# Performance work log

Measured on AMD Instinct MI355X. Metric: run time of the kernel, lower is better.

## Reference

```python
import jax, jax.numpy as jnp
import numpy as np

N_NODES = 100000
N_EDGES = 1600000
N_GRAPHS = 1024
HID = 128
FINAL = 128
SPATIAL = 3
NUM_LAYERS = 3
VOCAB = 100


def _linear_params(key, d_in, d_out):
    k1, k2 = jax.random.split(key)
    s = 1.0 / np.sqrt(d_in)
    W = jax.random.uniform(k1, (d_out, d_in), jnp.float32, -s, s)
    b = jax.random.uniform(k2, (d_out,), jnp.float32, -s, s)
    return W, b


def setup_inputs() -> dict:
    key = jax.random.key(0)
    ks = jax.random.split(key, 16)
    z = jax.random.randint(ks[0], (N_NODES,), 0, VOCAB)
    pos = jax.random.normal(ks[1], (N_NODES, SPATIAL), jnp.float32)
    edge_index = jax.random.randint(ks[2], (2, N_EDGES), 0, N_NODES)
    batch = jnp.sort(jax.random.randint(ks[3], (N_NODES,), 0, N_GRAPHS))
    emb_table = jax.random.normal(ks[4], (VOCAB, HID), jnp.float32)
    W_pos, b_pos = _linear_params(ks[5], SPATIAL, HID)
    W_comb, b_comb = _linear_params(ks[6], 2 * HID, HID)
    # GIN: each conv's MLP is Linear(d,d) -> ReLU -> Linear(d,d); all dims 128 here.
    gW1, gb1, gW2, gb2 = [], [], [], []
    for i in range(NUM_LAYERS):
        k = jax.random.fold_in(ks[7], i)
        ka, kb = jax.random.split(k)
        W1, b1 = _linear_params(ka, HID, HID)
        W2, b2 = _linear_params(kb, HID, FINAL if i == NUM_LAYERS - 1 else HID)
        gW1.append(W1); gb1.append(b1); gW2.append(W2); gb2.append(b2)
    gin_W1 = jnp.stack(gW1); gin_b1 = jnp.stack(gb1)
    gin_W2 = jnp.stack(gW2); gin_b2 = jnp.stack(gb2)
    W_p1, b_p1 = _linear_params(ks[8], FINAL, FINAL)
    W_p2, b_p2 = _linear_params(ks[9], FINAL, 1)
    return {
        "z": z, "pos": pos, "edge_index": edge_index, "batch": batch,
        "emb_table": emb_table, "W_pos": W_pos, "b_pos": b_pos,
        "W_comb": W_comb, "b_comb": b_comb,
        "gin_W1": gin_W1, "gin_b1": gin_b1, "gin_W2": gin_W2, "gin_b2": gin_b2,
        "W_p1": W_p1, "b_p1": b_p1, "W_p2": W_p2, "b_p2": b_p2,
    }


def reference(z, pos, edge_index, batch, emb_table, W_pos, b_pos, W_comb, b_comb,
              gin_W1, gin_b1, gin_W2, gin_b2, W_p1, b_p1, W_p2, b_p2):
    src, dst = edge_index[0], edge_index[1]
    # initial node embedding: embed(z) || linear(pos) -> linear -> relu
    atom = emb_table[z]                                   # [N, H]
    pe = pos @ W_pos.T + b_pos                            # [N, H]
    x = jax.nn.relu(jnp.concatenate([atom, pe], axis=-1) @ W_comb.T + b_comb)
    # GIN layers: x' = MLP((1+eps)*x + sum_{j->i} x_j), eps=0; act between convs only
    for i in range(NUM_LAYERS):
        aggr = jax.ops.segment_sum(x[src], dst, num_segments=N_NODES)  # [N, H]
        h = aggr + x
        h = jax.nn.relu(h @ gin_W1[i].T + gin_b1[i])
        x = h @ gin_W2[i].T + gin_b2[i]
        if i < NUM_LAYERS - 1:
            x = jax.nn.relu(x)
    # sum pooling per graph, then predict MLP
    g = jax.ops.segment_sum(x, batch, num_segments=N_GRAPHS)  # [G, F]
    h = jax.nn.relu(g @ W_p1.T + b_p1)
    return h @ W_p2.T + b_p2                              # [G, 1]
```

## Files before the change

### kernel.cpp

```cpp
#include <hip/hip_runtime.h>
#include <hip/hip_bf16.h>

#define HID 128
#define CAP 64
#define NBK 2048
#define NBL 1563

typedef __attribute__((ext_vector_type(8))) short bfrag;
typedef __attribute__((ext_vector_type(4))) float f32x4;

static inline size_t align256(size_t x) { return (x + 255) & ~(size_t)255; }

__device__ __forceinline__ unsigned short f2bf(float f) {
  unsigned int x = __float_as_uint(f);
  unsigned int r = x + 0x7fffu + ((x >> 16) & 1u);
  return (unsigned short)(r >> 16);
}
__device__ __forceinline__ float bflo(unsigned int u) { return __uint_as_float(u << 16); }
__device__ __forceinline__ float bfhi(unsigned int u) { return __uint_as_float(u & 0xffff0000u); }


__global__ __launch_bounds__(256) void k_prep(const int* __restrict__ src,
                                              const int* __restrict__ dst,
                                              int* __restrict__ cnt,
                                              int* __restrict__ bsrc, int E, int N,
                                              const float* __restrict__ W_comb,
                                              const float* __restrict__ gW1,
                                              const float* __restrict__ gW2,
                                              unsigned short* __restrict__ Wcb,
                                              unsigned short* __restrict__ W1b,
                                              unsigned short* __restrict__ W2b,
                                              const int* __restrict__ batch,
                                              int* __restrict__ goff, int G) {
  const int bid = blockIdx.x;
  const int tid = threadIdx.x;
  if (bid < NBK) {
    const int slice = bid & 7;
    const int sidx = bid >> 3;
    const int s_lo = (int)(((long long)slice * N) >> 3);
    const int s_hi = (int)(((long long)(slice + 1) * N) >> 3);
    for (int e = sidx * 256 + tid; e < E; e += (NBK / 8) * 256) {
      int d = dst[e];
      if (d >= s_lo && d < s_hi) {
        int slot = atomicAdd(&cnt[d], 1);
        if (slot < CAP) bsrc[(size_t)d * CAP + slot] = src[e];
      }
    }
  } else if (bid < NBK + 192) {
    int i = (bid - NBK) * 256 + tid;
    if (i < 128 * 256) Wcb[i] = f2bf(W_comb[i]);
    if (i < 3 * 128 * 128) {
      W1b[i] = f2bf(gW1[i]);
      W2b[i] = f2bf(gW2[i]);
    }
  } else {
    int g = (bid - NBK - 192) * 256 + tid;
    if (g <= G) {
      int lo = 0, hi = N;
      while (lo < hi) {
        int mid = (lo + hi) >> 1;
        if (batch[mid] < g) lo = mid + 1; else hi = mid;
      }
      goff[g] = lo;
    }
  }
}


__global__ __launch_bounds__(256, 2) void k_init_mm(const int* __restrict__ z,
                                                    const float* __restrict__ pos,
                                                    const float* __restrict__ emb,
                                                    const float* __restrict__ W_pos,
                                                    const float* __restrict__ b_pos,
                                                    const unsigned short* __restrict__ Wcb,
                                                    const float* __restrict__ bias,
                                                    const unsigned short* __restrict__ W1n,
                                                    unsigned short* __restrict__ Y, int n) {
  __shared__ unsigned int sE[32 * 128];
  __shared__ unsigned int sB[32 * 64];
  const int t = threadIdx.x;
  const int w = t >> 6, l = t & 63, lr = l & 15, lk = l >> 4;

  bfrag wcf[2][8];
#pragma unroll
  for (int s = 0; s < 2; ++s)
#pragma unroll
    for (int ks = 0; ks < 8; ++ks)
      wcf[s][ks] = *(const bfrag*)(Wcb + (size_t)(32 * w + 16 * s + lr) * 256 + ks * 32 + lk * 8);
  bfrag w1f[2][4];
#pragma unroll
  for (int s = 0; s < 2; ++s)
#pragma unroll
    for (int ks = 0; ks < 4; ++ks)
      w1f[s][ks] = *(const bfrag*)(W1n + (size_t)(32 * w + 16 * s + lr) * HID + ks * 32 + lk * 8);
  const float bias0 = bias[32 * w + lr];
  const float bias1 = bias[32 * w + 16 + lr];

  const int m0 = blockIdx.x * 32;
  {
    const int r = t >> 3, i = t & 7;
    int node = m0 + r;
    if (node >= n) node = n - 1;
    const int zz = z[node];
    const float p0 = pos[node * 3 + 0], p1 = pos[node * 3 + 1], p2 = pos[node * 3 + 2];
    const int swz = (r & 7) << 2;
#pragma unroll
    for (int k = 0; k < 16; ++k) {
      const int j = i + k * 8;
      float v0, v1;
      if (j < 64) {
        const float2 ev = *(const float2*)&emb[(size_t)zz * 128 + 2 * j];
        v0 = ev.x; v1 = ev.y;
      } else {
        const int f0 = 2 * j - 128;
        v0 = b_pos[f0] + W_pos[f0 * 3] * p0 + W_pos[f0 * 3 + 1] * p1 + W_pos[f0 * 3 + 2] * p2;
        v1 = b_pos[f0 + 1] + W_pos[f0 * 3 + 3] * p0 + W_pos[f0 * 3 + 4] * p1 +
             W_pos[f0 * 3 + 5] * p2;
      }
      sE[r * 128 + (j ^ swz)] = (unsigned int)f2bf(v0) | ((unsigned int)f2bf(v1) << 16);
    }
  }
  __syncthreads();

  f32x4 acc00 = {0.f, 0.f, 0.f, 0.f}, acc01 = acc00, acc10 = acc00, acc11 = acc00;
#pragma unroll
  for (int mt = 0; mt < 2; ++mt) {
    const int row = 16 * mt + lr;
    const int swz = (row & 7) << 2;
#pragma unroll
    for (int ks = 0; ks < 8; ++ks) {
      const bfrag a = *(const bfrag*)&sE[row * 128 + ((ks * 16 + lk * 4) ^ swz)];
      if (mt == 0) {
        acc00 = __builtin_amdgcn_mfma_f32_16x16x32_bf16(a, wcf[0][ks], acc00, 0, 0, 0);
        acc01 = __builtin_amdgcn_mfma_f32_16x16x32_bf16(a, wcf[1][ks], acc01, 0, 0, 0);
      } else {
        acc10 = __builtin_amdgcn_mfma_f32_16x16x32_bf16(a, wcf[0][ks], acc10, 0, 0, 0);
        acc11 = __builtin_amdgcn_mfma_f32_16x16x32_bf16(a, wcf[1][ks], acc11, 0, 0, 0);
      }
    }
  }
  {
    unsigned short* sB16 = (unsigned short*)sB;
#pragma unroll
    for (int mt = 0; mt < 2; ++mt) {
#pragma unroll
      for (int s = 0; s < 2; ++s) {
        const f32x4 a = mt == 0 ? (s == 0 ? acc00 : acc01) : (s == 0 ? acc10 : acc11);
        const float bb = s == 0 ? bias0 : bias1;
        const int col = 32 * w + 16 * s + lr;
#pragma unroll
        for (int r = 0; r < 4; ++r) {
          const int rowL = 16 * mt + 4 * lk + r;
          const int cu = (col >> 1) ^ ((rowL & 7) << 2);
          sB16[rowL * 128 + cu * 2 + (col & 1)] = f2bf(fmaxf(a[r] + bb, 0.f));
        }
      }
    }
  }
  __syncthreads();

  f32x4 u00 = {0.f, 0.f, 0.f, 0.f}, u01 = u00, u10 = u00, u11 = u00;
#pragma unroll
  for (int mt = 0; mt < 2; ++mt) {
    const int row = 16 * mt + lr;
    const int swz = (row & 7) << 2;
#pragma unroll
    for (int ks = 0; ks < 4; ++ks) {
      const bfrag a = *(const bfrag*)&sB[row * 64 + ((ks * 16 + lk * 4) ^ swz)];
      if (mt == 0) {
        u00 = __builtin_amdgcn_mfma_f32_16x16x32_bf16(a, w1f[0][ks], u00, 0, 0, 0);
        u01 = __builtin_amdgcn_mfma_f32_16x16x32_bf16(a, w1f[1][ks], u01, 0, 0, 0);
      } else {
        u10 = __builtin_amdgcn_mfma_f32_16x16x32_bf16(a, w1f[0][ks], u10, 0, 0, 0);
        u11 = __builtin_amdgcn_mfma_f32_16x16x32_bf16(a, w1f[1][ks], u11, 0, 0, 0);
      }
    }
  }
#pragma unroll
  for (int mt = 0; mt < 2; ++mt) {
#pragma unroll
    for (int s = 0; s < 2; ++s) {
      const f32x4 a = mt == 0 ? (s == 0 ? u00 : u01) : (s == 0 ? u10 : u11);
      const int col = 32 * w + 16 * s + lr;
#pragma unroll
      for (int r = 0; r < 4; ++r) {
        const int row = m0 + 16 * mt + 4 * lk + r;
        if (row < n) Y[(size_t)row * HID + col] = f2bf(a[r]);
      }
    }
  }
}


template <int LAST>
__global__ __launch_bounds__(256, 2) void k_layer(const unsigned int* __restrict__ U,
                                                  const int* __restrict__ cnt,
                                                  const int* __restrict__ bsrc,
                                                  const float* __restrict__ b1,
                                                  const unsigned short* __restrict__ W2b,
                                                  const float* __restrict__ b2,
                                                  const unsigned short* __restrict__ W1n,
                                                  unsigned short* __restrict__ Y, int n) {
  __shared__ unsigned int sA[32 * 64];
  __shared__ unsigned int sB[32 * 64];
  const int t = threadIdx.x;
  const int w = t >> 6, l = t & 63, lr = l & 15, lk = l >> 4;

  bfrag w2f[2][4];
#pragma unroll
  for (int s = 0; s < 2; ++s)
#pragma unroll
    for (int ks = 0; ks < 4; ++ks)
      w2f[s][ks] = *(const bfrag*)(W2b + (size_t)(32 * w + 16 * s + lr) * HID + ks * 32 + lk * 8);
  bfrag w1f[2][4];
  if (!LAST) {
#pragma unroll
    for (int s = 0; s < 2; ++s)
#pragma unroll
      for (int ks = 0; ks < 4; ++ks)
        w1f[s][ks] = *(const bfrag*)(W1n + (size_t)(32 * w + 16 * s + lr) * HID + ks * 32 + lk * 8);
  }
  const float b2a = b2[32 * w + lr];
  const float b2b = b2[32 * w + 16 + lr];
  const float2 b1v = *(const float2*)&b1[2 * l];

  const int ntiles = (n + 31) >> 5;
  for (int tile = blockIdx.x; tile < ntiles; tile += gridDim.x) {
    const int m0 = tile * 32;
#pragma unroll 1
    for (int ri = 0; ri < 8; ++ri) {
      const int row = 8 * w + ri;
      int node = m0 + row;
      if (node >= n) node = n - 1;
      int deg = cnt[node];
      if (deg > CAP) deg = CAP;
      const int eidx = bsrc[(size_t)node * CAP + l];
      const unsigned int us = U[(size_t)node * 64 + l];
      float s0[8], s1[8];
#pragma unroll
      for (int jj = 0; jj < 8; ++jj) { s0[jj] = 0.f; s1[jj] = 0.f; }
      s0[0] = bflo(us); s1[0] = bfhi(us);
      if (deg > 0) {
        for (int k = 0; k < deg; k += 8) {
#pragma unroll
          for (int jj = 0; jj < 8; ++jj) {
            const int kk = k + jj;
            const int lane = kk < deg ? kk : deg - 1;
            const int sidx = __shfl(eidx, lane);
            const unsigned int uu = U[(size_t)sidx * 64 + l];
            const float m = kk < deg ? 1.f : 0.f;
            s0[jj] += m * bflo(uu);
            s1[jj] += m * bfhi(uu);
          }
        }
      }
      const float r0 = ((s0[0] + s0[1]) + (s0[2] + s0[3])) + ((s0[4] + s0[5]) + (s0[6] + s0[7]));
      const float r1 = ((s1[0] + s1[1]) + (s1[2] + s1[3])) + ((s1[4] + s1[5]) + (s1[6] + s1[7]));
      sA[row * 64 + (l ^ ((row & 7) << 2))] =
          (unsigned int)f2bf(fmaxf(r0 + b1v.x, 0.f)) |
          ((unsigned int)f2bf(fmaxf(r1 + b1v.y, 0.f)) << 16);
    }
    __syncthreads();

    f32x4 acc00 = {0.f, 0.f, 0.f, 0.f}, acc01 = acc00, acc10 = acc00, acc11 = acc00;
#pragma unroll
    for (int mt = 0; mt < 2; ++mt) {
      const int row = 16 * mt + lr;
      const int swz = (row & 7) << 2;
#pragma unroll
      for (int ks = 0; ks < 4; ++ks) {
        const bfrag a = *(const bfrag*)&sA[row * 64 + ((ks * 16 + lk * 4) ^ swz)];
        if (mt == 0) {
          acc00 = __builtin_amdgcn_mfma_f32_16x16x32_bf16(a, w2f[0][ks], acc00, 0, 0, 0);
          acc01 = __builtin_amdgcn_mfma_f32_16x16x32_bf16(a, w2f[1][ks], acc01, 0, 0, 0);
        } else {
          acc10 = __builtin_amdgcn_mfma_f32_16x16x32_bf16(a, w2f[0][ks], acc10, 0, 0, 0);
          acc11 = __builtin_amdgcn_mfma_f32_16x16x32_bf16(a, w2f[1][ks], acc11, 0, 0, 0);
        }
      }
    }
    if (LAST) {
#pragma unroll
      for (int mt = 0; mt < 2; ++mt) {
#pragma unroll
        for (int s = 0; s < 2; ++s) {
          const f32x4 a = mt == 0 ? (s == 0 ? acc00 : acc01) : (s == 0 ? acc10 : acc11);
          const float bb = s == 0 ? b2a : b2b;
          const int col = 32 * w + 16 * s + lr;
#pragma unroll
          for (int r = 0; r < 4; ++r) {
            const int row = m0 + 16 * mt + 4 * lk + r;
            if (row < n) Y[(size_t)row * HID + col] = f2bf(a[r] + bb);
          }
        }
      }
      __syncthreads();
    } else {
      unsigned short* sB16 = (unsigned short*)sB;
#pragma unroll
      for (int mt = 0; mt < 2; ++mt) {
#pragma unroll
        for (int s = 0; s < 2; ++s) {
          const f32x4 a = mt == 0 ? (s == 0 ? acc00 : acc01) : (s == 0 ? acc10 : acc11);
          const float bb = s == 0 ? b2a : b2b;
          const int col = 32 * w + 16 * s + lr;
#pragma unroll
          for (int r = 0; r < 4; ++r) {
            const int rowL = 16 * mt + 4 * lk + r;
            const int cu = (col >> 1) ^ ((rowL & 7) << 2);
            sB16[rowL * 128 + cu * 2 + (col & 1)] = f2bf(fmaxf(a[r] + bb, 0.f));
          }
        }
      }
      __syncthreads();
      f32x4 u00 = {0.f, 0.f, 0.f, 0.f}, u01 = u00, u10 = u00, u11 = u00;
#pragma unroll
      for (int mt = 0; mt < 2; ++mt) {
        const int row = 16 * mt + lr;
        const int swz = (row & 7) << 2;
#pragma unroll
        for (int ks = 0; ks < 4; ++ks) {
          const bfrag a = *(const bfrag*)&sB[row * 64 + ((ks * 16 + lk * 4) ^ swz)];
          if (mt == 0) {
            u00 = __builtin_amdgcn_mfma_f32_16x16x32_bf16(a, w1f[0][ks], u00, 0, 0, 0);
            u01 = __builtin_amdgcn_mfma_f32_16x16x32_bf16(a, w1f[1][ks], u01, 0, 0, 0);
          } else {
            u10 = __builtin_amdgcn_mfma_f32_16x16x32_bf16(a, w1f[0][ks], u10, 0, 0, 0);
            u11 = __builtin_amdgcn_mfma_f32_16x16x32_bf16(a, w1f[1][ks], u11, 0, 0, 0);
          }
        }
      }
#pragma unroll
      for (int mt = 0; mt < 2; ++mt) {
#pragma unroll
        for (int s = 0; s < 2; ++s) {
          const f32x4 a = mt == 0 ? (s == 0 ? u00 : u01) : (s == 0 ? u10 : u11);
          const int col = 32 * w + 16 * s + lr;
#pragma unroll
          for (int r = 0; r < 4; ++r) {
            const int row = m0 + 16 * mt + 4 * lk + r;
            if (row < n) Y[(size_t)row * HID + col] = f2bf(a[r]);
          }
        }
      }
    }
  }
}


__global__ __launch_bounds__(128) void k_pool(const unsigned short* __restrict__ X,
                                              const int* __restrict__ goff,
                                              const float* __restrict__ Wp1,
                                              const float* __restrict__ bp1,
                                              const float* __restrict__ Wp2,
                                              const float* __restrict__ bp2,
                                              float* __restrict__ out, int G) {
  __shared__ float sg[HID];
  __shared__ float sred[HID];
  int g = blockIdx.x;
  int f = threadIdx.x;
  int n0 = goff[g], n1 = goff[g + 1];
  float c0 = 0.f, c1 = 0.f, c2 = 0.f, c3 = 0.f;
  int nn = n0;
  for (; nn + 3 < n1; nn += 4) {
    c0 += __uint_as_float((unsigned int)X[(size_t)nn * HID + f] << 16);
    c1 += __uint_as_float((unsigned int)X[(size_t)(nn + 1) * HID + f] << 16);
    c2 += __uint_as_float((unsigned int)X[(size_t)(nn + 2) * HID + f] << 16);
    c3 += __uint_as_float((unsigned int)X[(size_t)(nn + 3) * HID + f] << 16);
  }
  for (; nn < n1; ++nn) c0 += __uint_as_float((unsigned int)X[(size_t)nn * HID + f] << 16);
  sg[f] = (c0 + c1) + (c2 + c3);
  __syncthreads();
  float a0 = 0.f, a1 = 0.f, a2 = 0.f, a3 = 0.f;
#pragma unroll
  for (int k4 = 0; k4 < 32; ++k4) {
    float4 wv = *(const float4*)&Wp1[f * HID + k4 * 4];
    float4 xv = *(const float4*)&sg[k4 * 4];
    a0 += wv.x * xv.x; a1 += wv.y * xv.y; a2 += wv.z * xv.z; a3 += wv.w * xv.w;
  }
  float h = fmaxf(bp1[f] + ((a0 + a1) + (a2 + a3)), 0.f);
  sred[f] = Wp2[f] * h;
  __syncthreads();
  for (int s = 64; s > 0; s >>= 1) {
    if (f < s) sred[f] += sred[f + s];
    __syncthreads();
  }
  if (f == 0) out[g] = sred[0] + bp2[0];
}


extern "C" void kernel_launch(void* const* d_in, const int* in_sizes, int n_in,
                              void* d_out, int out_size, void* d_ws, size_t ws_size,
                              hipStream_t stream) {
  const int*   z      = (const int*)d_in[0];
  const float* pos    = (const float*)d_in[1];
  const int*   ei     = (const int*)d_in[2];
  const int*   batch  = (const int*)d_in[3];
  const float* emb    = (const float*)d_in[4];
  const float* W_pos  = (const float*)d_in[5];
  const float* b_pos  = (const float*)d_in[6];
  const float* W_comb = (const float*)d_in[7];
  const float* b_comb = (const float*)d_in[8];
  const float* gW1    = (const float*)d_in[9];
  const float* gb1    = (const float*)d_in[10];
  const float* gW2    = (const float*)d_in[11];
  const float* gb2    = (const float*)d_in[12];
  const float* Wp1    = (const float*)d_in[13];
  const float* bp1    = (const float*)d_in[14];
  const float* Wp2    = (const float*)d_in[15];
  const float* bp2    = (const float*)d_in[16];
  float* out = (float*)d_out;

  const int N = in_sizes[0];
  const int E = in_sizes[2] / 2;
  const int G = out_size;
  const int* srcp = ei;
  const int* dstp = ei + E;

  char* w = (char*)d_ws;
  unsigned short* Ub  = (unsigned short*)w; w += align256((size_t)N * 128 * 2);
  unsigned short* Vb  = (unsigned short*)w; w += align256((size_t)N * 128 * 2);
  unsigned short* Wcb = (unsigned short*)w; w += align256((size_t)128 * 256 * 2);
  unsigned short* W1b = (unsigned short*)w; w += align256((size_t)3 * 128 * 128 * 2);
  unsigned short* W2b = (unsigned short*)w; w += align256((size_t)3 * 128 * 128 * 2);
  int* cnt  = (int*)w; w += align256((size_t)N * 4);
  int* bsrc = (int*)w; w += align256((size_t)N * CAP * 4);
  int* goff = (int*)w; w += align256((size_t)(G + 1) * 4);

  hipMemsetAsync(cnt, 0, (size_t)N * 4, stream);

  k_prep<<<NBK + 192 + 5, 256, 0, stream>>>(srcp, dstp, cnt, bsrc, E, N,
                                            W_comb, gW1, gW2, Wcb, W1b, W2b,
                                            batch, goff, G);

  k_init_mm<<<(N + 31) / 32, 256, 0, stream>>>(z, pos, emb, W_pos, b_pos, Wcb, b_comb,
                                               W1b, Ub, N);

  k_layer<0><<<NBL, 256, 0, stream>>>((const unsigned int*)Ub, cnt, bsrc, gb1,
                                      W2b, gb2, W1b + (size_t)1 * 128 * 128, Vb, N);
  k_layer<0><<<NBL, 256, 0, stream>>>((const unsigned int*)Vb, cnt, bsrc, gb1 + 128,
                                      W2b + (size_t)1 * 128 * 128, gb2 + 128,
                                      W1b + (size_t)2 * 128 * 128, Ub, N);
  k_layer<1><<<NBL, 256, 0, stream>>>((const unsigned int*)Ub, cnt, bsrc, gb1 + 256,
                                      W2b + (size_t)2 * 128 * 128, gb2 + 256,
                                      (const unsigned short*)nullptr, Vb, N);

  k_pool<<<G, HID, 0, stream>>>(Vb, goff, Wp1, bp1, Wp2, bp2, out, G);
}
```

Before: 476.6 us.

## Vectorize neighbor gather with 16-byte loads and four edges per wave

The aggregation loop now has each wave split into four lane groups of 16. Each lane loads a 16-byte uint4 of the bf16 row, so one wave gathers four neighbor rows per instruction, and partial sums are reduced with xor shuffles. Degrees and edge indices for all eight rows are prefetched up front. The persistent grid-stride tile loop is replaced by one block per 32-row tile, and the occupancy hint is raised from 2 to 3 blocks per CU. This targets the latency of many 4-byte scattered gathers, at the cost of extra shuffle reductions and higher register pressure.

```diff
diff --git a/kernel.cpp b/kernel.cpp
--- a/kernel.cpp
+++ b/kernel.cpp
@@ -4,7 +4,6 @@
 #define HID 128
 #define CAP 64
 #define NBK 2048
-#define NBL 1563
 
 typedef __attribute__((ext_vector_type(8))) short bfrag;
 typedef __attribute__((ext_vector_type(4))) float f32x4;
@@ -193,7 +192,7 @@
 
 
 template <int LAST>
-__global__ __launch_bounds__(256, 2) void k_layer(const unsigned int* __restrict__ U,
+__global__ __launch_bounds__(256, 3) void k_layer(const unsigned int* __restrict__ U,
                                                   const int* __restrict__ cnt,
                                                   const int* __restrict__ bsrc,
                                                   const float* __restrict__ b1,
@@ -205,6 +204,7 @@
   __shared__ unsigned int sB[32 * 64];
   const int t = threadIdx.x;
   const int w = t >> 6, l = t & 63, lr = l & 15, lk = l >> 4;
+  const int lgrp = lk, lpos = lr;
 
   bfrag w2f[2][4];
 #pragma unroll
@@ -222,125 +222,155 @@
   }
   const float b2a = b2[32 * w + lr];
   const float b2b = b2[32 * w + 16 + lr];
-  const float2 b1v = *(const float2*)&b1[2 * l];
-
-  const int ntiles = (n + 31) >> 5;
-  for (int tile = blockIdx.x; tile < ntiles; tile += gridDim.x) {
-    const int m0 = tile * 32;
-#pragma unroll 1
-    for (int ri = 0; ri < 8; ++ri) {
-      const int row = 8 * w + ri;
-      int node = m0 + row;
-      if (node >= n) node = n - 1;
-      int deg = cnt[node];
-      if (deg > CAP) deg = CAP;
-      const int eidx = bsrc[(size_t)node * CAP + l];
-      const unsigned int us = U[(size_t)node * 64 + l];
-      float s0[8], s1[8];
-#pragma unroll
-      for (int jj = 0; jj < 8; ++jj) { s0[jj] = 0.f; s1[jj] = 0.f; }
-      s0[0] = bflo(us); s1[0] = bfhi(us);
-      if (deg > 0) {
-        for (int k = 0; k < deg; k += 8) {
-#pragma unroll
-          for (int jj = 0; jj < 8; ++jj) {
-            const int kk = k + jj;
-            const int lane = kk < deg ? kk : deg - 1;
-            const int sidx = __shfl(eidx, lane);
-            const unsigned int uu = U[(size_t)sidx * 64 + l];
-            const float m = kk < deg ? 1.f : 0.f;
-            s0[jj] += m * bflo(uu);
-            s1[jj] += m * bfhi(uu);
-          }
+  const float4 bb0 = *(const float4*)&b1[8 * lpos];
+  const float4 bb1 = *(const float4*)&b1[8 * lpos + 4];
+  const float ms = (lgrp == 0) ? 1.f : 0.f;
+
+  const int m0 = blockIdx.x * 32;
+
+  int degs[8];
+  int eidxs[8];
+#pragma unroll
+  for (int ri = 0; ri < 8; ++ri) {
+    int node = m0 + 8 * w + ri;
+    if (node >= n) node = n - 1;
+    int d = cnt[node];
+    degs[ri] = d > CAP ? CAP : d;
+    eidxs[ri] = bsrc[(size_t)node * CAP + l];
+  }
+#pragma unroll
+  for (int ri = 0; ri < 8; ++ri) {
+    const int row = 8 * w + ri;
+    int node = m0 + row;
+    if (node >= n) node = n - 1;
+    const int deg = degs[ri];
+    const int eidx = eidxs[ri];
+    const uint4 sv = *(const uint4*)(U + (size_t)node * 64 + 4 * lpos);
+    float a0 = ms * bflo(sv.x), a1 = ms * bfhi(sv.x);
+    float a2 = ms * bflo(sv.y), a3 = ms * bfhi(sv.y);
+    float a4 = ms * bflo(sv.z), a5 = ms * bfhi(sv.z);
+    float a6 = ms * bflo(sv.w), a7 = ms * bfhi(sv.w);
+    int k = 0;
+    for (; k + 7 < deg; k += 8) {
+      const int e0 = __shfl(eidx, k + lgrp);
+      const int e1 = __shfl(eidx, k + 4 + lgrp);
+      const uint4 u0 = *(const uint4*)(U + (size_t)e0 * 64 + 4 * lpos);
+      const uint4 u1 = *(const uint4*)(U + (size_t)e1 * 64 + 4 * lpos);
+      a0 += bflo(u0.x); a1 += bfhi(u0.x); a2 += bflo(u0.y); a3 += bfhi(u0.y);
+      a4 += bflo(u0.z); a5 += bfhi(u0.z); a6 += bflo(u0.w); a7 += bfhi(u0.w);
+      a0 += bflo(u1.x); a1 += bfhi(u1.x); a2 += bflo(u1.y); a3 += bfhi(u1.y);
+      a4 += bflo(u1.z); a5 += bfhi(u1.z); a6 += bflo(u1.w); a7 += bfhi(u1.w);
+    }
+    for (; k < deg; k += 4) {
+      int idx = k + lgrp;
+      const float m = idx < deg ? 1.f : 0.f;
+      if (idx >= deg) idx = deg - 1;
+      const int e0 = __shfl(eidx, idx);
+      const uint4 u0 = *(const uint4*)(U + (size_t)e0 * 64 + 4 * lpos);
+      a0 += m * bflo(u0.x); a1 += m * bfhi(u0.x); a2 += m * bflo(u0.y); a3 += m * bfhi(u0.y);
+      a4 += m * bflo(u0.z); a5 += m * bfhi(u0.z); a6 += m * bflo(u0.w); a7 += m * bfhi(u0.w);
+    }
+    a0 += __shfl_xor(a0, 16); a0 += __shfl_xor(a0, 32);
+    a1 += __shfl_xor(a1, 16); a1 += __shfl_xor(a1, 32);
+    a2 += __shfl_xor(a2, 16); a2 += __shfl_xor(a2, 32);
+    a3 += __shfl_xor(a3, 16); a3 += __shfl_xor(a3, 32);
+    a4 += __shfl_xor(a4, 16); a4 += __shfl_xor(a4, 32);
+    a5 += __shfl_xor(a5, 16); a5 += __shfl_xor(a5, 32);
+    a6 += __shfl_xor(a6, 16); a6 += __shfl_xor(a6, 32);
+    a7 += __shfl_xor(a7, 16); a7 += __shfl_xor(a7, 32);
+    if (lgrp == 0) {
+      const int swz = (row & 7) << 2;
+      uint4 o;
+      o.x = (unsigned int)f2bf(fmaxf(a0 + bb0.x, 0.f)) |
+            ((unsigned int)f2bf(fmaxf(a1 + bb0.y, 0.f)) << 16);
+      o.y = (unsigned int)f2bf(fmaxf(a2 + bb0.z, 0.f)) |
+            ((unsigned int)f2bf(fmaxf(a3 + bb0.w, 0.f)) << 16);
+      o.z = (unsigned int)f2bf(fmaxf(a4 + bb1.x, 0.f)) |
+            ((unsigned int)f2bf(fmaxf(a5 + bb1.y, 0.f)) << 16);
+      o.w = (unsigned int)f2bf(fmaxf(a6 + bb1.z, 0.f)) |
+            ((unsigned int)f2bf(fmaxf(a7 + bb1.w, 0.f)) << 16);
+      *(uint4*)&sA[row * 64 + ((4 * lpos) ^ swz)] = o;
+    }
+  }
+  __syncthreads();
+
+  f32x4 acc00 = {0.f, 0.f, 0.f, 0.f}, acc01 = acc00, acc10 = acc00, acc11 = acc00;
+#pragma unroll
+  for (int mt = 0; mt < 2; ++mt) {
+    const int row = 16 * mt + lr;
+    const int swz = (row & 7) << 2;
+#pragma unroll
+    for (int ks = 0; ks < 4; ++ks) {
+      const bfrag a = *(const bfrag*)&sA[row * 64 + ((ks * 16 + lk * 4) ^ swz)];
+      if (mt == 0) {
+        acc00 = __builtin_amdgcn_mfma_f32_16x16x32_bf16(a, w2f[0][ks], acc00, 0, 0, 0);
+        acc01 = __builtin_amdgcn_mfma_f32_16x16x32_bf16(a, w2f[1][ks], acc01, 0, 0, 0);
+      } else {
+        acc10 = __builtin_amdgcn_mfma_f32_16x16x32_bf16(a, w2f[0][ks], acc10, 0, 0, 0);
+        acc11 = __builtin_amdgcn_mfma_f32_16x16x32_bf16(a, w2f[1][ks], acc11, 0, 0, 0);
+      }
+    }
+  }
+  if (LAST) {
+#pragma unroll
+    for (int mt = 0; mt < 2; ++mt) {
+#pragma unroll
+      for (int s = 0; s < 2; ++s) {
+        const f32x4 a = mt == 0 ? (s == 0 ? acc00 : acc01) : (s == 0 ? acc10 : acc11);
+        const float bb = s == 0 ? b2a : b2b;
+        const int col = 32 * w + 16 * s + lr;
+#pragma unroll
+        for (int r = 0; r < 4; ++r) {
+          const int row = m0 + 16 * mt + 4 * lk + r;
+          if (row < n) Y[(size_t)row * HID + col] = f2bf(a[r] + bb);
         }
       }
-      const float r0 = ((s0[0] + s0[1]) + (s0[2] + s0[3])) + ((s0[4] + s0[5]) + (s0[6] + s0[7]));
-      const float r1 = ((s1[0] + s1[1]) + (s1[2] + s1[3])) + ((s1[4] + s1[5]) + (s1[6] + s1[7]));
-      sA[row * 64 + (l ^ ((row & 7) << 2))] =
-          (unsigned int)f2bf(fmaxf(r0 + b1v.x, 0.f)) |
-          ((unsigned int)f2bf(fmaxf(r1 + b1v.y, 0.f)) << 16);
+    }
+  } else {
+    unsigned short* sB16 = (unsigned short*)sB;
+#pragma unroll
+    for (int mt = 0; mt < 2; ++mt) {
+#pragma unroll
+      for (int s = 0; s < 2; ++s) {
+        const f32x4 a = mt == 0 ? (s == 0 ? acc00 : acc01) : (s == 0 ? acc10 : acc11);
+        const float bb = s == 0 ? b2a : b2b;
+        const int col = 32 * w + 16 * s + lr;
+#pragma unroll
+        for (int r = 0; r < 4; ++r) {
+          const int rowL = 16 * mt + 4 * lk + r;
+          const int cu = (col >> 1) ^ ((rowL & 7) << 2);
+          sB16[rowL * 128 + cu * 2 + (col & 1)] = f2bf(fmaxf(a[r] + bb, 0.f));
+        }
+      }
     }
     __syncthreads();
-
-    f32x4 acc00 = {0.f, 0.f, 0.f, 0.f}, acc01 = acc00, acc10 = acc00, acc11 = acc00;
+    f32x4 u00 = {0.f, 0.f, 0.f, 0.f}, u01 = u00, u10 = u00, u11 = u00;
 #pragma unroll
     for (int mt = 0; mt < 2; ++mt) {
       const int row = 16 * mt + lr;
       const int swz = (row & 7) << 2;
 #pragma unroll
       for (int ks = 0; ks < 4; ++ks) {
-        const bfrag a = *(const bfrag*)&sA[row * 64 + ((ks * 16 + lk * 4) ^ swz)];
+        const bfrag a = *(const bfrag*)&sB[row * 64 + ((ks * 16 + lk * 4) ^ swz)];
         if (mt == 0) {
-          acc00 = __builtin_amdgcn_mfma_f32_16x16x32_bf16(a, w2f[0][ks], acc00, 0, 0, 0);
-          acc01 = __builtin_amdgcn_mfma_f32_16x16x32_bf16(a, w2f[1][ks], acc01, 0, 0, 0);
+          u00 = __builtin_amdgcn_mfma_f32_16x16x32_bf16(a, w1f[0][ks], u00, 0, 0, 0);
+          u01 = __builtin_amdgcn_mfma_f32_16x16x32_bf16(a, w1f[1][ks], u01, 0, 0, 0);
         } else {
-          acc10 = __builtin_amdgcn_mfma_f32_16x16x32_bf16(a, w2f[0][ks], acc10, 0, 0, 0);
-          acc11 = __builtin_amdgcn_mfma_f32_16x16x32_bf16(a, w2f[1][ks], acc11, 0, 0, 0);
+          u10 = __builtin_amdgcn_mfma_f32_16x16x32_bf16(a, w1f[0][ks], u10, 0, 0, 0);
+          u11 = __builtin_amdgcn_mfma_f32_16x16x32_bf16(a, w1f[1][ks], u11, 0, 0, 0);
         }
       }
     }
-    if (LAST) {
-#pragma unroll
-      for (int mt = 0; mt < 2; ++mt) {
-#pragma unroll
-        for (int s = 0; s < 2; ++s) {
-          const f32x4 a = mt == 0 ? (s == 0 ? acc00 : acc01) : (s == 0 ? acc10 : acc11);
-          const float bb = s == 0 ? b2a : b2b;
-          const int col = 32 * w + 16 * s + lr;
-#pragma unroll
-          for (int r = 0; r < 4; ++r) {
-            const int row = m0 + 16 * mt + 4 * lk + r;
-            if (row < n) Y[(size_t)row * HID + col] = f2bf(a[r] + bb);
-          }
-        }
-      }
-      __syncthreads();
-    } else {
-      unsigned short* sB16 = (unsigned short*)sB;
-#pragma unroll
-      for (int mt = 0; mt < 2; ++mt) {
-#pragma unroll
-        for (int s = 0; s < 2; ++s) {
-          const f32x4 a = mt == 0 ? (s == 0 ? acc00 : acc01) : (s == 0 ? acc10 : acc11);
-          const float bb = s == 0 ? b2a : b2b;
-          const int col = 32 * w + 16 * s + lr;
-#pragma unroll
-          for (int r = 0; r < 4; ++r) {
-            const int rowL = 16 * mt + 4 * lk + r;
-            const int cu = (col >> 1) ^ ((rowL & 7) << 2);
-            sB16[rowL * 128 + cu * 2 + (col & 1)] = f2bf(fmaxf(a[r] + bb, 0.f));
-          }
-        }
-      }
-      __syncthreads();
-      f32x4 u00 = {0.f, 0.f, 0.f, 0.f}, u01 = u00, u10 = u00, u11 = u00;
-#pragma unroll
-      for (int mt = 0; mt < 2; ++mt) {
-        const int row = 16 * mt + lr;
-        const int swz = (row & 7) << 2;
-#pragma unroll
-        for (int ks = 0; ks < 4; ++ks) {
-          const bfrag a = *(const bfrag*)&sB[row * 64 + ((ks * 16 + lk * 4) ^ swz)];
-          if (mt == 0) {
-            u00 = __builtin_amdgcn_mfma_f32_16x16x32_bf16(a, w1f[0][ks], u00, 0, 0, 0);
-            u01 = __builtin_amdgcn_mfma_f32_16x16x32_bf16(a, w1f[1][ks], u01, 0, 0, 0);
-          } else {
-            u10 = __builtin_amdgcn_mfma_f32_16x16x32_bf16(a, w1f[0][ks], u10, 0, 0, 0);
-            u11 = __builtin_amdgcn_mfma_f32_16x16x32_bf16(a, w1f[1][ks], u11, 0, 0, 0);
-          }
-        }
-      }
-#pragma unroll
-      for (int mt = 0; mt < 2; ++mt) {
-#pragma unroll
-        for (int s = 0; s < 2; ++s) {
-          const f32x4 a = mt == 0 ? (s == 0 ? u00 : u01) : (s == 0 ? u10 : u11);
-          const int col = 32 * w + 16 * s + lr;
-#pragma unroll
-          for (int r = 0; r < 4; ++r) {
-            const int row = m0 + 16 * mt + 4 * lk + r;
-            if (row < n) Y[(size_t)row * HID + col] = f2bf(a[r]);
-          }
+#pragma unroll
+    for (int mt = 0; mt < 2; ++mt) {
+#pragma unroll
+      for (int s = 0; s < 2; ++s) {
+        const f32x4 a = mt == 0 ? (s == 0 ? u00 : u01) : (s == 0 ? u10 : u11);
+        const int col = 32 * w + 16 * s + lr;
+#pragma unroll
+        for (int r = 0; r < 4; ++r) {
+          const int row = m0 + 16 * mt + 4 * lk + r;
+          if (row < n) Y[(size_t)row * HID + col] = f2bf(a[r]);
         }
       }
     }
@@ -416,6 +446,7 @@
   const int G = out_size;
   const int* srcp = ei;
   const int* dstp = ei + E;
+  const int ntiles = (N + 31) / 32;
 
   char* w = (char*)d_ws;
   unsigned short* Ub  = (unsigned short*)w; w += align256((size_t)N * 128 * 2);
@@ -433,17 +464,17 @@
                                             W_comb, gW1, gW2, Wcb, W1b, W2b,
                                             batch, goff, G);
 
-  k_init_mm<<<(N + 31) / 32, 256, 0, stream>>>(z, pos, emb, W_pos, b_pos, Wcb, b_comb,
-                                               W1b, Ub, N);
-
-  k_layer<0><<<NBL, 256, 0, stream>>>((const unsigned int*)Ub, cnt, bsrc, gb1,
-                                      W2b, gb2, W1b + (size_t)1 * 128 * 128, Vb, N);
-  k_layer<0><<<NBL, 256, 0, stream>>>((const unsigned int*)Vb, cnt, bsrc, gb1 + 128,
-                                      W2b + (size_t)1 * 128 * 128, gb2 + 128,
-                                      W1b + (size_t)2 * 128 * 128, Ub, N);
-  k_layer<1><<<NBL, 256, 0, stream>>>((const unsigned int*)Ub, cnt, bsrc, gb1 + 256,
-                                      W2b + (size_t)2 * 128 * 128, gb2 + 256,
-                                      (const unsigned short*)nullptr, Vb, N);
+  k_init_mm<<<ntiles, 256, 0, stream>>>(z, pos, emb, W_pos, b_pos, Wcb, b_comb,
+                                        W1b, Ub, N);
+
+  k_layer<0><<<ntiles, 256, 0, stream>>>((const unsigned int*)Ub, cnt, bsrc, gb1,
+                                         W2b, gb2, W1b + (size_t)1 * 128 * 128, Vb, N);
+  k_layer<0><<<ntiles, 256, 0, stream>>>((const unsigned int*)Vb, cnt, bsrc, gb1 + 128,
+                                         W2b + (size_t)1 * 128 * 128, gb2 + 128,
+                                         W1b + (size_t)2 * 128 * 128, Ub, N);
+  k_layer<1><<<ntiles, 256, 0, stream>>>((const unsigned int*)Ub, cnt, bsrc, gb1 + 256,
+                                         W2b + (size_t)2 * 128 * 128, gb2 + 256,
+                                         (const unsigned short*)nullptr, Vb, N);
 
   k_pool<<<G, HID, 0, stream>>>(Vb, goff, Wp1, bp1, Wp2, bp2, out, G);
 }
```

After: 431.9 us. 9.4% less time.
